# Performance work log

Hardware: AMD Instinct MI355X
Metric: run time of the kernel (lower is better)

## Reference

```python
import jax, jax.numpy as jnp
import numpy as np

PAST = 12
FUTURE = 12
INPUT_SIZE = 256
OUTPUT_SIZE = FUTURE * INPUT_SIZE  # 3072


def setup_inputs() -> dict:
    key = jax.random.key(0)
    k_inp, k_w, k_b = jax.random.split(key, 3)
    inp = jax.random.normal(k_inp, (64, 288, INPUT_SIZE), dtype=jnp.float32)
    fan_in = INPUT_SIZE * PAST
    bound = 1.0 / np.sqrt(fan_in)
    # torch nn.Linear init: U(-1/sqrt(fan_in), 1/sqrt(fan_in)); W is (out, in)
    W = jax.random.uniform(k_w, (OUTPUT_SIZE, fan_in), minval=-bound, maxval=bound, dtype=jnp.float32)
    b = jax.random.uniform(k_b, (OUTPUT_SIZE,), minval=-bound, maxval=bound, dtype=jnp.float32)
    return {"inp": inp, "W": W, "b": b}


def reference(inp, W, b):
    batch, length, dim = inp.shape
    n_win = length - PAST  # number of sliding windows (torch loop count)
    # Gather all overlapping windows at once: (batch, n_win, PAST, dim)
    idx = jnp.arange(n_win)[:, None] + jnp.arange(PAST)[None, :]
    windows = inp[:, idx, :].reshape(batch, n_win, PAST * dim)
    # One batched GEMM replaces n_win tiny Linear calls: x @ W.T + b
    out = jnp.einsum('bnk,ok->bno', windows, W) + b
    return out.reshape(batch, -1, FUTURE, dim)
```

## Files before the change

kernel.cpp:

```cpp
#include <hip/hip_runtime.h>
#include <hip/hip_bf16.h>

#define BATCH   64
#define LEN     288
#define DIM     256
#define PAST    12
#define NWIN    (LEN - PAST)
#define M_DIM   (BATCH * NWIN)
#define K_DIM   (PAST * DIM)
#define N_DIM   3072

#define BM 256
#define BN 256
#define BK 64
#define NTILE   (K_DIM / BK)
#define NITER   (NTILE / 2)

#define GRID_N   12
#define BULK_WG  768
#define TAIL_M0  16384
#define TAIL_QN  24
#define TAIL_WG  240

typedef __attribute__((ext_vector_type(8))) short bh8;
typedef __attribute__((ext_vector_type(4))) float f32x4;

__device__ __forceinline__ void llds16(const void* g, void* l) {
    __builtin_amdgcn_global_load_lds(
        (const __attribute__((address_space(1))) unsigned int*)g,
        (__attribute__((address_space(3))) unsigned int*)l,
        16, 0, 0);
}

__global__ void cvt_f32_bf16(const float* __restrict__ in,
                             __hip_bfloat16* __restrict__ out, int n8) {
    int i = blockIdx.x * blockDim.x + threadIdx.x;
    if (i >= n8) return;
    const float4* p = (const float4*)in;
    float4 a = p[2 * i], b = p[2 * i + 1];
    union { __hip_bfloat16 h[8]; int4 v; } u;
    u.h[0] = __float2bfloat16(a.x); u.h[1] = __float2bfloat16(a.y);
    u.h[2] = __float2bfloat16(a.z); u.h[3] = __float2bfloat16(a.w);
    u.h[4] = __float2bfloat16(b.x); u.h[5] = __float2bfloat16(b.y);
    u.h[6] = __float2bfloat16(b.z); u.h[7] = __float2bfloat16(b.w);
    ((int4*)out)[i] = u.v;
}

#define PH_MID  __builtin_amdgcn_s_barrier(); __builtin_amdgcn_s_setprio(1);
#define PH_END  __builtin_amdgcn_s_setprio(0); __builtin_amdgcn_s_barrier();
#define PH_END_VM(N) __builtin_amdgcn_s_setprio(0); \
                asm volatile("s_waitcnt vmcnt(" #N ")" ::: "memory"); \
                __builtin_amdgcn_s_barrier();

#define LDS_A(buf) (smem + (buf) * 65536)
#define LDS_B(buf) (smem + (buf) * 65536 + 32768)

#define RD_A4(buf, MB) { \
    const char* _b = LDS_A(buf) + aRowB; \
    _Pragma("unroll") for (int mi = 0; mi < 4; ++mi) { \
        a0[mi][0] = *(const bh8*)(_b + (MB + mi) * 2048 + kOff0); \
        a0[mi][1] = *(const bh8*)(_b + (MB + mi) * 2048 + kOff1); \
    } }
#define RD_B2(buf, dst, NB) { \
    const char* _b = LDS_B(buf) + bRowB; \
    _Pragma("unroll") for (int ni = 0; ni < 2; ++ni) { \
        dst[ni][0] = *(const bh8*)(_b + (NB + ni) * 2048 + kOff0); \
        dst[ni][1] = *(const bh8*)(_b + (NB + ni) * 2048 + kOff1); \
    } }
#define MFMA_Q(MB, NB, BB) \
    _Pragma("unroll") for (int mi = 0; mi < 4; ++mi) \
    _Pragma("unroll") for (int ni = 0; ni < 2; ++ni) { \
        acc[MB + mi][NB + ni] = __builtin_amdgcn_mfma_f32_16x16x32_bf16( \
            a0[mi][0], BB[ni][0], acc[MB + mi][NB + ni], 0, 0, 0); \
        acc[MB + mi][NB + ni] = __builtin_amdgcn_mfma_f32_16x16x32_bf16( \
            a0[mi][1], BB[ni][1], acc[MB + mi][NB + ni], 0, 0, 0); \
    }
#define STG_A1(buf, kt, q) \
    llds16(Ag + aSrc[q] + (kt) * 64, LDS_A(buf) + (q) * 8192 + wOff);
#define STG_B1(buf, kt, u) \
    llds16(Wg + bSrc[u] + (kt) * 64, LDS_B(buf) + (u) * 8192 + wOff);

__global__ __launch_bounds__(512, 2)
void gemm_bulk(const __hip_bfloat16* __restrict__ Ag,
               const __hip_bfloat16* __restrict__ Wg,
               const float* __restrict__ bias,
               float* __restrict__ C)
{
    extern __shared__ char smem[];

    const int tid = threadIdx.x;
    const int wgid = (blockIdx.x & 7) * (BULK_WG / 8) + (blockIdx.x >> 3);
    const int bm = wgid / GRID_N;
    const int bn = wgid - bm * GRID_N;
    const int tile_m = bm * BM;
    const int tile_n = bn * BN;

    const int rd  = tid >> 3;
    const int chs = (((tid & 7) ^ (rd & 7)) * 8);
    int aSrc[4], bSrc[4];
#pragma unroll
    for (int rb = 0; rb < 4; ++rb) {
        int m  = tile_m + rb * 64 + rd;
        int bq = m / NWIN;
        int wq = m - bq * NWIN;
        aSrc[rb] = (bq * LEN + wq) * DIM + chs;
        bSrc[rb] = (tile_n + rb * 64 + rd) * K_DIM + chs;
    }

    const int wave = tid >> 6, lane = tid & 63;
    const int wm = wave >> 2, wn = wave & 3;
    const int fr = lane & 15, kg = lane >> 4;
    const int sw    = (fr & 7) << 4;
    const int kOff0 = (kg * 16) ^ sw;
    const int kOff1 = kOff0 ^ 64;
    const int aRowB = (wm * 128 + fr) * 128;
    const int bRowB = (wn * 64 + fr) * 128;
    const int wOff  = wave * 1024;

    bh8 a0[4][2], fb0[2][2], fb1[2][2];
    f32x4 acc[8][4] = {};

    STG_A1(0, 0, 0); STG_A1(0, 0, 1); STG_A1(0, 0, 2); STG_A1(0, 0, 3);
    STG_B1(0, 0, 0); STG_B1(0, 0, 1); STG_B1(0, 0, 2); STG_B1(0, 0, 3);
    STG_A1(1, 1, 0); STG_A1(1, 1, 2);
    STG_B1(1, 1, 0); STG_B1(1, 1, 1);
    STG_A1(1, 1, 1); STG_A1(1, 1, 3);
    asm volatile("s_waitcnt vmcnt(6)" ::: "memory");
    __builtin_amdgcn_s_barrier();

#pragma unroll 1
    for (int it = 0; it < NITER; ++it) {
        const int b = 2 * it + 1;
        int c = 2 * it + 2; if (c >= NTILE) c = NTILE - 2;
        int d = 2 * it + 3; if (d >= NTILE) d = NTILE - 1;

        RD_B2(0, fb0, 0); RD_A4(0, 0);
        STG_B1(1, b, 2); STG_B1(1, b, 3);
        PH_MID; MFMA_Q(0, 0, fb0); PH_END;

        RD_B2(0, fb1, 2);
        STG_A1(0, c, 0); STG_A1(0, c, 2);
        PH_MID; MFMA_Q(0, 2, fb1); PH_END;

        RD_A4(0, 4);
        STG_B1(0, c, 0); STG_B1(0, c, 1);
        PH_MID; MFMA_Q(4, 2, fb1); PH_END;

        STG_A1(0, c, 1); STG_A1(0, c, 3);
        PH_MID; MFMA_Q(4, 0, fb0); PH_END_VM(6);

        RD_B2(1, fb0, 0); RD_A4(1, 0);
        STG_B1(0, c, 2); STG_B1(0, c, 3);
        PH_MID; MFMA_Q(0, 0, fb0); PH_END;

        RD_B2(1, fb1, 2);
        STG_A1(1, d, 0); STG_A1(1, d, 2);
        PH_MID; MFMA_Q(0, 2, fb1); PH_END;

        RD_A4(1, 4);
        STG_B1(1, d, 0); STG_B1(1, d, 1);
        PH_MID; MFMA_Q(4, 2, fb1); PH_END;

        STG_A1(1, d, 1); STG_A1(1, d, 3);
        PH_MID; MFMA_Q(4, 0, fb0); PH_END_VM(6);
    }

    float bv[4];
    const float* bp = bias + tile_n + wn * 64 + fr;
#pragma unroll
    for (int ni = 0; ni < 4; ++ni) bv[ni] = bp[ni * 16];

    const int r0 = (lane >> 4) * 4;
#pragma unroll
    for (int mi = 0; mi < 8; ++mi) {
#pragma unroll
        for (int j = 0; j < 4; ++j) {
            long m = tile_m + wm * 128 + mi * 16 + r0 + j;
            float* crow = C + m * (long)N_DIM + tile_n + wn * 64 + fr;
#pragma unroll
            for (int ni = 0; ni < 4; ++ni)
                __builtin_nontemporal_store(acc[mi][ni][j] + bv[ni], &crow[ni * 16]);
        }
    }
}

#define TLDS_A(buf) (smem + (buf) * 32768)
#define TLDS_B(buf) (smem + (buf) * 32768 + 16384)

#define T_RD(buf) { \
    const char* _bb = TLDS_B(buf) + bRowB; \
    _Pragma("unroll") for (int ni = 0; ni < 2; ++ni) { \
        fb0[ni][0] = *(const bh8*)(_bb + ni * 2048 + kOff0); \
        fb0[ni][1] = *(const bh8*)(_bb + ni * 2048 + kOff1); \
    } \
    const char* _a = TLDS_A(buf) + aRowB; \
    _Pragma("unroll") for (int mi = 0; mi < 4; ++mi) { \
        a0[mi][0] = *(const bh8*)(_a + mi * 2048 + kOff0); \
        a0[mi][1] = *(const bh8*)(_a + mi * 2048 + kOff1); \
    } }
#define T_MFMA(MB) \
    _Pragma("unroll") for (int mi = 0; mi < 2; ++mi) \
    _Pragma("unroll") for (int ni = 0; ni < 2; ++ni) { \
        acc[MB + mi][ni] = __builtin_amdgcn_mfma_f32_16x16x32_bf16( \
            a0[MB + mi][0], fb0[ni][0], acc[MB + mi][ni], 0, 0, 0); \
        acc[MB + mi][ni] = __builtin_amdgcn_mfma_f32_16x16x32_bf16( \
            a0[MB + mi][1], fb0[ni][1], acc[MB + mi][ni], 0, 0, 0); \
    }
#define T_STG_A(buf, kt, u) \
    llds16(Ag + aSrc[u] + (kt) * 64, TLDS_A(buf) + (u) * 8192 + wOff);
#define T_STG_B(buf, kt, u) \
    llds16(Wg + bSrc[u] + (kt) * 64, TLDS_B(buf) + (u) * 8192 + wOff);

__global__ __launch_bounds__(512, 2)
void gemm_tail(const __hip_bfloat16* __restrict__ Ag,
               const __hip_bfloat16* __restrict__ Wg,
               const float* __restrict__ bias,
               float* __restrict__ C)
{
    extern __shared__ char smem[];

    const int tid = threadIdx.x;
    const int wgid = (blockIdx.x & 7) * (TAIL_WG / 8) + (blockIdx.x >> 3);
    const int qm = wgid / TAIL_QN;
    const int qn = wgid - qm * TAIL_QN;
    const int tile_m = TAIL_M0 + qm * 128;
    const int tile_n = qn * 128;

    const int rd  = tid >> 3;
    const int chs = (((tid & 7) ^ (rd & 7)) * 8);
    int aSrc[2], bSrc[2];
#pragma unroll
    for (int rb = 0; rb < 2; ++rb) {
        int m  = tile_m + rb * 64 + rd;
        int bq = m / NWIN;
        int wq = m - bq * NWIN;
        aSrc[rb] = (bq * LEN + wq) * DIM + chs;
        bSrc[rb] = (tile_n + rb * 64 + rd) * K_DIM + chs;
    }

    const int wave = tid >> 6, lane = tid & 63;
    const int wm = wave >> 2, wn = wave & 3;
    const int fr = lane & 15, kg = lane >> 4;
    const int sw    = (fr & 7) << 4;
    const int kOff0 = (kg * 16) ^ sw;
    const int kOff1 = kOff0 ^ 64;
    const int aRowB = (wm * 64 + fr) * 128;
    const int bRowB = (wn * 32 + fr) * 128;
    const int wOff  = wave * 1024;

    bh8 a0[4][2], fb0[2][2];
    f32x4 acc[4][2] = {};

    T_STG_A(0, 0, 0); T_STG_A(0, 0, 1); T_STG_B(0, 0, 0); T_STG_B(0, 0, 1);
    T_STG_A(1, 1, 0); T_STG_A(1, 1, 1);
    asm volatile("s_waitcnt vmcnt(2)" ::: "memory");
    __builtin_amdgcn_s_barrier();

#pragma unroll 1
    for (int it = 0; it < NITER; ++it) {
        const int b = 2 * it + 1;
        int c = 2 * it + 2; if (c >= NTILE) c = NTILE - 2;
        int d = 2 * it + 3; if (d >= NTILE) d = NTILE - 1;

        T_RD(0);
        T_STG_B(1, b, 0); T_STG_B(1, b, 1);
        PH_MID; T_MFMA(0); PH_END;

        T_STG_A(0, c, 0); T_STG_A(0, c, 1);
        PH_MID; T_MFMA(2); PH_END_VM(2);

        T_RD(1);
        T_STG_B(0, c, 0); T_STG_B(0, c, 1);
        PH_MID; T_MFMA(0); PH_END;

        T_STG_A(1, d, 0); T_STG_A(1, d, 1);
        PH_MID; T_MFMA(2); PH_END_VM(2);
    }

    float bv[2];
    const float* bp = bias + tile_n + wn * 32 + fr;
#pragma unroll
    for (int ni = 0; ni < 2; ++ni) bv[ni] = bp[ni * 16];

    const int r0 = (lane >> 4) * 4;
#pragma unroll
    for (int mi = 0; mi < 4; ++mi) {
#pragma unroll
        for (int j = 0; j < 4; ++j) {
            long m = tile_m + wm * 64 + mi * 16 + r0 + j;
            float* crow = C + m * (long)N_DIM + tile_n + wn * 32 + fr;
#pragma unroll
            for (int ni = 0; ni < 2; ++ni)
                __builtin_nontemporal_store(acc[mi][ni][j] + bv[ni], &crow[ni * 16]);
        }
    }
}

extern "C" void kernel_launch(void* const* d_in, const int* in_sizes, int n_in,
                              void* d_out, int out_size, void* d_ws, size_t ws_size,
                              hipStream_t stream) {
    const float* inp  = (const float*)d_in[0];
    const float* Wf   = (const float*)d_in[1];
    const float* bias = (const float*)d_in[2];
    float* out = (float*)d_out;

    __hip_bfloat16* Abf = (__hip_bfloat16*)d_ws;
    __hip_bfloat16* Wbf = (__hip_bfloat16*)((char*)d_ws + (size_t)BATCH * LEN * DIM * 2);

    const int nA8 = BATCH * LEN * DIM / 8;
    const int nW8 = N_DIM * K_DIM / 8;
    cvt_f32_bf16<<<(nA8 + 255) / 256, 256, 0, stream>>>(inp, Abf, nA8);
    cvt_f32_bf16<<<(nW8 + 255) / 256, 256, 0, stream>>>(Wf, Wbf, nW8);

    hipFuncSetAttribute((const void*)gemm_bulk,
                        hipFuncAttributeMaxDynamicSharedMemorySize, 131072);
    hipFuncSetAttribute((const void*)gemm_tail,
                        hipFuncAttributeMaxDynamicSharedMemorySize, 65536);
    gemm_bulk<<<dim3(BULK_WG), 512, 131072, stream>>>(Abf, Wbf, bias, out);
    gemm_tail<<<dim3(TAIL_WG), 512, 65536, stream>>>(Abf, Wbf, bias, out);
}
```

Before: 309.8 us.

## Restructure bulk GEMM pipeline with triple-buffered B and fused bf16 conversion

The bulk GEMM main loop changes from four quarter-phases per K tile to two half-phases. A stays double-buffered, B becomes triple-buffered and is prefetched two tiles ahead, and all four B fragments are read at once. sched_barrier fences are placed around the s_barriers to pin instruction order. The two fp32-to-bf16 conversion launches become one kernel. The cost is more dynamic LDS (160 KB, about the whole CU's LDS on this part) and more fragment registers, which could hurt occupancy or spill.

```diff
diff --git a/kernel.cpp b/kernel.cpp
--- a/kernel.cpp
+++ b/kernel.cpp
@@ -14,7 +14,6 @@
 #define BN 256
 #define BK 64
 #define NTILE   (K_DIM / BK)
-#define NITER   (NTILE / 2)
 
 #define GRID_N   12
 #define BULK_WG  768
@@ -32,53 +31,77 @@
         16, 0, 0);
 }
 
-__global__ void cvt_f32_bf16(const float* __restrict__ in,
-                             __hip_bfloat16* __restrict__ out, int n8) {
+__global__ void cvt_both(const float* __restrict__ inA, const float* __restrict__ inW,
+                         __hip_bfloat16* __restrict__ outA, __hip_bfloat16* __restrict__ outW,
+                         int nA8, int nTot8) {
     int i = blockIdx.x * blockDim.x + threadIdx.x;
-    if (i >= n8) return;
-    const float4* p = (const float4*)in;
-    float4 a = p[2 * i], b = p[2 * i + 1];
+    if (i >= nTot8) return;
+    const float* src;
+    __hip_bfloat16* dst;
+    int k;
+    if (i < nA8) { src = inA; dst = outA; k = i; }
+    else         { src = inW; dst = outW; k = i - nA8; }
+    const float4* p = (const float4*)src;
+    float4 a = p[2 * k], b = p[2 * k + 1];
     union { __hip_bfloat16 h[8]; int4 v; } u;
     u.h[0] = __float2bfloat16(a.x); u.h[1] = __float2bfloat16(a.y);
     u.h[2] = __float2bfloat16(a.z); u.h[3] = __float2bfloat16(a.w);
     u.h[4] = __float2bfloat16(b.x); u.h[5] = __float2bfloat16(b.y);
     u.h[6] = __float2bfloat16(b.z); u.h[7] = __float2bfloat16(b.w);
-    ((int4*)out)[i] = u.v;
-}
-
-#define PH_MID  __builtin_amdgcn_s_barrier(); __builtin_amdgcn_s_setprio(1);
-#define PH_END  __builtin_amdgcn_s_setprio(0); __builtin_amdgcn_s_barrier();
-#define PH_END_VM(N) __builtin_amdgcn_s_setprio(0); \
+    ((int4*)dst)[k] = u.v;
+}
+
+#define SB0 __builtin_amdgcn_sched_barrier(0)
+#define PH_MID  SB0; __builtin_amdgcn_s_barrier(); SB0; __builtin_amdgcn_s_setprio(1);
+#define PH_END  __builtin_amdgcn_s_setprio(0); SB0; __builtin_amdgcn_s_barrier(); SB0;
+#define PH_END_VM(N) __builtin_amdgcn_s_setprio(0); SB0; \
                 asm volatile("s_waitcnt vmcnt(" #N ")" ::: "memory"); \
-                __builtin_amdgcn_s_barrier();
-
-#define LDS_A(buf) (smem + (buf) * 65536)
-#define LDS_B(buf) (smem + (buf) * 65536 + 32768)
-
-#define RD_A4(buf, MB) { \
-    const char* _b = LDS_A(buf) + aRowB; \
+                __builtin_amdgcn_s_barrier(); SB0;
+
+#define ALDS(r) (smem + (r) * 32768)
+#define BLDS(r) (smem + 65536 + (r) * 32768)
+
+#define RD_FB(r) { \
+    const char* _b = BLDS(r) + bRowB; \
+    _Pragma("unroll") for (int ni = 0; ni < 4; ++ni) { \
+        fb[ni][0] = *(const bh8*)(_b + ni * 2048 + kOff0); \
+        fb[ni][1] = *(const bh8*)(_b + ni * 2048 + kOff1); \
+    } }
+#define RD_A(r, MB) { \
+    const char* _b = ALDS(r) + aRowB; \
     _Pragma("unroll") for (int mi = 0; mi < 4; ++mi) { \
-        a0[mi][0] = *(const bh8*)(_b + (MB + mi) * 2048 + kOff0); \
-        a0[mi][1] = *(const bh8*)(_b + (MB + mi) * 2048 + kOff1); \
+        a0[mi][0] = *(const bh8*)(_b + ((MB) + mi) * 2048 + kOff0); \
+        a0[mi][1] = *(const bh8*)(_b + ((MB) + mi) * 2048 + kOff1); \
     } }
-#define RD_B2(buf, dst, NB) { \
-    const char* _b = LDS_B(buf) + bRowB; \
-    _Pragma("unroll") for (int ni = 0; ni < 2; ++ni) { \
-        dst[ni][0] = *(const bh8*)(_b + (NB + ni) * 2048 + kOff0); \
-        dst[ni][1] = *(const bh8*)(_b + (NB + ni) * 2048 + kOff1); \
-    } }
-#define MFMA_Q(MB, NB, BB) \
+#define MFMA_PH(MB) \
     _Pragma("unroll") for (int mi = 0; mi < 4; ++mi) \
-    _Pragma("unroll") for (int ni = 0; ni < 2; ++ni) { \
-        acc[MB + mi][NB + ni] = __builtin_amdgcn_mfma_f32_16x16x32_bf16( \
-            a0[mi][0], BB[ni][0], acc[MB + mi][NB + ni], 0, 0, 0); \
-        acc[MB + mi][NB + ni] = __builtin_amdgcn_mfma_f32_16x16x32_bf16( \
-            a0[mi][1], BB[ni][1], acc[MB + mi][NB + ni], 0, 0, 0); \
-    }
-#define STG_A1(buf, kt, q) \
-    llds16(Ag + aSrc[q] + (kt) * 64, LDS_A(buf) + (q) * 8192 + wOff);
-#define STG_B1(buf, kt, u) \
-    llds16(Wg + bSrc[u] + (kt) * 64, LDS_B(buf) + (u) * 8192 + wOff);
+    _Pragma("unroll") for (int ni = 0; ni < 4; ++ni) { \
+        acc[(MB) + mi][ni] = __builtin_amdgcn_mfma_f32_16x16x32_bf16( \
+            a0[mi][0], fb[ni][0], acc[(MB) + mi][ni], 0, 0, 0); \
+        acc[(MB) + mi][ni] = __builtin_amdgcn_mfma_f32_16x16x32_bf16( \
+            a0[mi][1], fb[ni][1], acc[(MB) + mi][ni], 0, 0, 0); \
+    }
+#define STG_A4(r, kt) { \
+    llds16(Ag + aSrc[0] + (kt) * 64, ALDS(r) + 0 * 8192 + wOff); \
+    llds16(Ag + aSrc[1] + (kt) * 64, ALDS(r) + 1 * 8192 + wOff); \
+    llds16(Ag + aSrc[2] + (kt) * 64, ALDS(r) + 2 * 8192 + wOff); \
+    llds16(Ag + aSrc[3] + (kt) * 64, ALDS(r) + 3 * 8192 + wOff); }
+#define STG_B4(r, kt) { \
+    llds16(Wg + bSrc[0] + (kt) * 64, BLDS(r) + 0 * 8192 + wOff); \
+    llds16(Wg + bSrc[1] + (kt) * 64, BLDS(r) + 1 * 8192 + wOff); \
+    llds16(Wg + bSrc[2] + (kt) * 64, BLDS(r) + 2 * 8192 + wOff); \
+    llds16(Wg + bSrc[3] + (kt) * 64, BLDS(r) + 3 * 8192 + wOff); }
+
+#define TILE(t, r2, r3, ra2, rn3) { \
+    const int _tA = ((t) + 1 < NTILE) ? (t) + 1 : NTILE - 1; \
+    const int _tB = ((t) + 2 < NTILE) ? (t) + 2 : NTILE - 1; \
+    RD_FB(r3); RD_A(r2, 0); \
+    STG_A4(ra2, _tA); \
+    PH_MID; MFMA_PH(0); PH_END; \
+    RD_A(r2, 4); \
+    STG_B4(rn3, _tB); \
+    PH_MID; MFMA_PH(4); PH_END_VM(4); \
+}
 
 __global__ __launch_bounds__(512, 2)
 void gemm_bulk(const __hip_bfloat16* __restrict__ Ag,
@@ -117,52 +140,25 @@
     const int bRowB = (wn * 64 + fr) * 128;
     const int wOff  = wave * 1024;
 
-    bh8 a0[4][2], fb0[2][2], fb1[2][2];
+    bh8 a0[4][2], fb[4][2];
     f32x4 acc[8][4] = {};
 
-    STG_A1(0, 0, 0); STG_A1(0, 0, 1); STG_A1(0, 0, 2); STG_A1(0, 0, 3);
-    STG_B1(0, 0, 0); STG_B1(0, 0, 1); STG_B1(0, 0, 2); STG_B1(0, 0, 3);
-    STG_A1(1, 1, 0); STG_A1(1, 1, 2);
-    STG_B1(1, 1, 0); STG_B1(1, 1, 1);
-    STG_A1(1, 1, 1); STG_A1(1, 1, 3);
-    asm volatile("s_waitcnt vmcnt(6)" ::: "memory");
+    STG_B4(0, 0);
+    STG_A4(0, 0);
+    STG_B4(1, 1);
+    asm volatile("s_waitcnt vmcnt(4)" ::: "memory");
     __builtin_amdgcn_s_barrier();
+    SB0;
 
 #pragma unroll 1
-    for (int it = 0; it < NITER; ++it) {
-        const int b = 2 * it + 1;
-        int c = 2 * it + 2; if (c >= NTILE) c = NTILE - 2;
-        int d = 2 * it + 3; if (d >= NTILE) d = NTILE - 1;
-
-        RD_B2(0, fb0, 0); RD_A4(0, 0);
-        STG_B1(1, b, 2); STG_B1(1, b, 3);
-        PH_MID; MFMA_Q(0, 0, fb0); PH_END;
-
-        RD_B2(0, fb1, 2);
-        STG_A1(0, c, 0); STG_A1(0, c, 2);
-        PH_MID; MFMA_Q(0, 2, fb1); PH_END;
-
-        RD_A4(0, 4);
-        STG_B1(0, c, 0); STG_B1(0, c, 1);
-        PH_MID; MFMA_Q(4, 2, fb1); PH_END;
-
-        STG_A1(0, c, 1); STG_A1(0, c, 3);
-        PH_MID; MFMA_Q(4, 0, fb0); PH_END_VM(6);
-
-        RD_B2(1, fb0, 0); RD_A4(1, 0);
-        STG_B1(0, c, 2); STG_B1(0, c, 3);
-        PH_MID; MFMA_Q(0, 0, fb0); PH_END;
-
-        RD_B2(1, fb1, 2);
-        STG_A1(1, d, 0); STG_A1(1, d, 2);
-        PH_MID; MFMA_Q(0, 2, fb1); PH_END;
-
-        RD_A4(1, 4);
-        STG_B1(1, d, 0); STG_B1(1, d, 1);
-        PH_MID; MFMA_Q(4, 2, fb1); PH_END;
-
-        STG_A1(1, d, 1); STG_A1(1, d, 3);
-        PH_MID; MFMA_Q(4, 0, fb0); PH_END_VM(6);
+    for (int j = 0; j < NTILE / 6; ++j) {
+        const int t = 6 * j;
+        TILE(t + 0, 0, 0, 1, 2);
+        TILE(t + 1, 1, 1, 0, 0);
+        TILE(t + 2, 0, 2, 1, 1);
+        TILE(t + 3, 1, 0, 0, 2);
+        TILE(t + 4, 0, 1, 1, 0);
+        TILE(t + 5, 1, 2, 0, 1);
     }
 
     float bv[4];
@@ -255,9 +251,10 @@
     T_STG_A(1, 1, 0); T_STG_A(1, 1, 1);
     asm volatile("s_waitcnt vmcnt(2)" ::: "memory");
     __builtin_amdgcn_s_barrier();
+    SB0;
 
 #pragma unroll 1
-    for (int it = 0; it < NITER; ++it) {
+    for (int it = 0; it < NTILE / 2; ++it) {
         const int b = 2 * it + 1;
         int c = 2 * it + 2; if (c >= NTILE) c = NTILE - 2;
         int d = 2 * it + 3; if (d >= NTILE) d = NTILE - 1;
@@ -309,13 +306,13 @@
 
     const int nA8 = BATCH * LEN * DIM / 8;
     const int nW8 = N_DIM * K_DIM / 8;
-    cvt_f32_bf16<<<(nA8 + 255) / 256, 256, 0, stream>>>(inp, Abf, nA8);
-    cvt_f32_bf16<<<(nW8 + 255) / 256, 256, 0, stream>>>(Wf, Wbf, nW8);
+    const int nT8 = nA8 + nW8;
+    cvt_both<<<(nT8 + 255) / 256, 256, 0, stream>>>(inp, Wf, Abf, Wbf, nA8, nT8);
 
     hipFuncSetAttribute((const void*)gemm_bulk,
-                        hipFuncAttributeMaxDynamicSharedMemorySize, 131072);
+                        hipFuncAttributeMaxDynamicSharedMemorySize, 163840);
     hipFuncSetAttribute((const void*)gemm_tail,
                         hipFuncAttributeMaxDynamicSharedMemorySize, 65536);
-    gemm_bulk<<<dim3(BULK_WG), 512, 131072, stream>>>(Abf, Wbf, bias, out);
+    gemm_bulk<<<dim3(BULK_WG), 512, 163840, stream>>>(Abf, Wbf, bias, out);
     gemm_tail<<<dim3(TAIL_WG), 512, 65536, stream>>>(Abf, Wbf, bias, out);
 }
```

Result: slower. 329.4 us (+6.3%).
